# Optimization experiments

Hardware: AMD Instinct MI355X
Metric: run time of the kernel (lower is better)

The kernel has to match this reference:

```python
import jax, jax.numpy as jnp
import numpy as np

N_NODES = 50000
NEG_SLOPE = 0.2

def _segment_softmax(e, seg, n):
    m = jax.ops.segment_max(e, seg, num_segments=n)
    ex = jnp.exp(e - m[seg])
    s = jax.ops.segment_sum(ex, seg, num_segments=n)
    return ex / s[seg]

def _gatv2_layer(x, src, dst, n, Wl, bl, Wr, br, att):
    # GATv2 (heads=1): e_ij = att . leaky_relu(Wl x_j + Wr x_i); msg = alpha * Wl x_j
    xl = x @ Wl + bl            # [N, D] source transform
    xr = x @ Wr + br            # [N, D] target transform
    h = jax.nn.leaky_relu(xl[src] + xr[dst], NEG_SLOPE)  # [E, D]
    e = h @ att                 # [E]
    alpha = _segment_softmax(e, dst, n)
    out = jax.ops.segment_sum(alpha[:, None] * xl[src], dst, num_segments=n)
    return out

def setup_inputs() -> dict:
    key = jax.random.key(0)
    ks = jax.random.split(key, 16)
    N, E, Q, F, D, H = N_NODES, 800000, 200000, 128, 250, 256
    def glorot(k, shape):
        fan = shape[0] + shape[-1]
        return jax.random.uniform(k, shape, jnp.float32, -1.0, 1.0) * np.sqrt(6.0 / fan)
    return {
        "x": jax.random.normal(ks[0], (N, F), jnp.float32),
        "edge_index": jax.random.randint(ks[1], (2, E), 0, N, jnp.int32),
        "query": jax.random.randint(ks[2], (Q, 2), 0, N, jnp.int32),
        "W1l": glorot(ks[3], (F, D)), "b1l": jnp.zeros((D,), jnp.float32),
        "W1r": glorot(ks[4], (F, D)), "b1r": jnp.zeros((D,), jnp.float32),
        "att1": glorot(ks[5], (D,)),
        "W2l": glorot(ks[6], (D, D)), "b2l": jnp.zeros((D,), jnp.float32),
        "W2r": glorot(ks[7], (D, D)), "b2r": jnp.zeros((D,), jnp.float32),
        "att2": glorot(ks[8], (D,)),
        "Wm1": glorot(ks[9], (2 * D, H)), "bm1": jnp.zeros((H,), jnp.float32),
        "Wm2": glorot(ks[10], (H, 1)), "bm2": jnp.zeros((1,), jnp.float32),
    }

def reference(x, edge_index, query, W1l, b1l, W1r, b1r, att1,
              W2l, b2l, W2r, b2r, att2, Wm1, bm1, Wm2, bm2):
    n = x.shape[0]
    # add self loops (PyG default add_self_loops=True)
    loops = jnp.arange(n, dtype=edge_index.dtype)
    src = jnp.concatenate([edge_index[0], loops])
    dst = jnp.concatenate([edge_index[1], loops])
    h = _gatv2_layer(x, src, dst, n, W1l, b1l, W1r, b1r, att1)
    h = jax.nn.relu(h)
    emb = _gatv2_layer(h, src, dst, n, W2l, b2l, W2r, b2r, att2)
    # edge-prediction head: gather pair embeddings, concat, MLP
    pair = jnp.concatenate([emb[query[:, 0]], emb[query[:, 1]]], axis=1)  # [Q, 2D]
    out = jax.nn.relu(pair @ Wm1 + bm1)
    out = jax.nn.relu(out @ Wm2 + bm2)
    return out
```

## Files before the change

kernel.cpp:

```cpp
#include <hip/hip_runtime.h>
#include <hip/hip_fp16.h>
#include <math.h>
#include <stdint.h>

#define NN 50000
#define NE 800000
#define ET (NE + NN)
#define FIN 128
#define DD 250
#define HD 256
#define NQ 200000
#define NEG_SLOPE 0.2f

typedef unsigned short u16;
typedef __attribute__((ext_vector_type(4))) float f32x4;
typedef _Float16 h2v __attribute__((ext_vector_type(2)));
typedef _Float16 f16x8 __attribute__((ext_vector_type(8)));

union H2U { h2v h; unsigned int u; };

__device__ __forceinline__ u16 f2h(float v) {
    __half h = __float2half(v);
    return *reinterpret_cast<u16*>(&h);
}
__device__ __forceinline__ float4 ld4h(const u16* p) {
    uint2 r = *(const uint2*)p;
    __half2 a = *(__half2*)&r.x;
    __half2 b = *(__half2*)&r.y;
    float2 fa = __half22float2(a), fb = __half22float2(b);
    return make_float4(fa.x, fa.y, fb.x, fb.y);
}
__device__ __forceinline__ h2v hmax2v(h2v a, h2v b) {
    return __builtin_elementwise_max(a, b);
}


#define DPPMOV(v, ctrl, rm) \
    ((unsigned int)__builtin_amdgcn_update_dpp(0, (int)(v), (ctrl), (rm), 0xF, true))

__device__ __forceinline__ unsigned int h2_wave_sum63(h2v x) {
    H2U u, t; u.h = x;
    t.u = DPPMOV(u.u, 0x111, 0xF); u.h = u.h + t.h;
    t.u = DPPMOV(u.u, 0x112, 0xF); u.h = u.h + t.h;
    t.u = DPPMOV(u.u, 0x114, 0xF); u.h = u.h + t.h;
    t.u = DPPMOV(u.u, 0x118, 0xF); u.h = u.h + t.h;
    t.u = DPPMOV(u.u, 0x142, 0xA); u.h = u.h + t.h;
    t.u = DPPMOV(u.u, 0x143, 0xC); u.h = u.h + t.h;
    return (unsigned int)__builtin_amdgcn_readlane((int)u.u, 63);
}

__device__ __forceinline__ float f32_wave_sum63(float x) {
    union FU { float f; unsigned int u; } a, t, o;
    a.f = x;
    t.u = DPPMOV(a.u, 0x111, 0xF); a.f += t.f;
    t.u = DPPMOV(a.u, 0x112, 0xF); a.f += t.f;
    t.u = DPPMOV(a.u, 0x114, 0xF); a.f += t.f;
    t.u = DPPMOV(a.u, 0x118, 0xF); a.f += t.f;
    t.u = DPPMOV(a.u, 0x142, 0xA); a.f += t.f;
    t.u = DPPMOV(a.u, 0x143, 0xC); a.f += t.f;
    o.u = (unsigned int)__builtin_amdgcn_readlane((int)a.u, 63);
    return o.f;
}


__global__ void count_kernel(const int* __restrict__ ei, int* __restrict__ cnt) {
    int k = blockIdx.x * 256 + threadIdx.x;
    if (k >= ET) return;
    int d = (k < NE) ? ei[NE + k] : (k - NE);
    atomicAdd(&cnt[d], 1);
}

__global__ __launch_bounds__(256) void scan1_kernel(
    int* __restrict__ cnt, int* __restrict__ rowptr, int* __restrict__ bsum)
{
    __shared__ int buf[256];
    int t = threadIdx.x;
    int i = blockIdx.x * 256 + t;
    int v = (i < NN) ? cnt[i] : 0;
    if (i < NN) cnt[i] = 0;
    buf[t] = v;
    __syncthreads();
#pragma unroll
    for (int off = 1; off < 256; off <<= 1) {
        int add = (t >= off) ? buf[t - off] : 0;
        __syncthreads();
        buf[t] += add;
        __syncthreads();
    }
    if (i < NN) rowptr[i] = buf[t] - v;
    if (t == 255) bsum[blockIdx.x] = buf[255];
}

__global__ __launch_bounds__(256) void scan2_kernel(
    int* __restrict__ bsum, int* __restrict__ rowptr, int nb)
{
    __shared__ int buf[256];
    int t = threadIdx.x;
    int v = (t < nb) ? bsum[t] : 0;
    buf[t] = v;
    __syncthreads();
#pragma unroll
    for (int off = 1; off < 256; off <<= 1) {
        int add = (t >= off) ? buf[t - off] : 0;
        __syncthreads();
        buf[t] += add;
        __syncthreads();
    }
    if (t < nb) bsum[t] = buf[t] - v;
    if (t == 255) rowptr[NN] = buf[255];
}

__global__ __launch_bounds__(256) void scan3_kernel(
    int* __restrict__ rowptr, const int* __restrict__ bsum)
{
    int i = blockIdx.x * 256 + threadIdx.x;
    if (i < NN) rowptr[i] += bsum[blockIdx.x];
}

__global__ void scatter_kernel(const int* __restrict__ ei,
                               const int* __restrict__ rowptr,
                               int* __restrict__ fill,
                               int* __restrict__ ssrc) {
    int k = blockIdx.x * 256 + threadIdx.x;
    if (k >= ET) return;
    int s, d;
    if (k < NE) { s = ei[k]; d = ei[NE + k]; }
    else        { s = k - NE; d = k - NE; }
    int pos = rowptr[d] + atomicAdd(&fill[d], 1);
    ssrc[pos] = s << 9;
}


#define CONVX_BLOCKS 3125

__global__ __launch_bounds__(256) void conv_all(
    const float* __restrict__ x, int* __restrict__ fill,
    u16* __restrict__ Asp,
    const float* __restrict__ W1l, const float* __restrict__ W1r,
    const float* __restrict__ W2l, const float* __restrict__ W2r,
    const float* __restrict__ Wm1,
    u16* __restrict__ W1lT, u16* __restrict__ W1rT,
    u16* __restrict__ W2lT, u16* __restrict__ W2rT,
    u16* __restrict__ WmtT, u16* __restrict__ WmbT)
{
    if (blockIdx.x < CONVX_BLOCKS) {
        int tid = blockIdx.x * 256 + threadIdx.x;
        if (tid < NN) fill[tid] = 0;
        size_t idx = (size_t)tid * 8;
        if (idx >= (size_t)NN * FIN) return;
        float4 v0 = *(const float4*)(x + idx);
        float4 v1 = *(const float4*)(x + idx + 4);
        ushort4 o0, o1;
        o0.x = f2h(v0.x); o0.y = f2h(v0.y); o0.z = f2h(v0.z); o0.w = f2h(v0.w);
        o1.x = f2h(v1.x); o1.y = f2h(v1.y); o1.z = f2h(v1.z); o1.w = f2h(v1.w);
        *(ushort4*)(Asp + idx) = o0;
        *(ushort4*)(Asp + idx + 4) = o1;
        return;
    }
    int b = blockIdx.x - CONVX_BLOCKS;
    const float* W; int K, N, koff, kshift, b0; u16* ot;
    if (b < 128)       { W = W1l; K = FIN; N = DD; koff = 0;  kshift = 7; b0 = 0;    ot = W1lT; }
    else if (b < 256)  { W = W1r; K = FIN; N = DD; koff = 0;  kshift = 7; b0 = 128;  ot = W1rT; }
    else if (b < 512)  { W = W2l; K = DD;  N = DD; koff = 0;  kshift = 8; b0 = 256;  ot = W2lT; }
    else if (b < 768)  { W = W2r; K = DD;  N = DD; koff = 0;  kshift = 8; b0 = 512;  ot = W2rT; }
    else if (b < 1024) { W = Wm1; K = DD;  N = HD; koff = 0;  kshift = 8; b0 = 768;  ot = WmtT; }
    else               { W = Wm1; K = DD;  N = HD; koff = DD; kshift = 8; b0 = 1024; ot = WmbT; }
    int id = (b - b0) * 256 + threadIdx.x;
    int Kp = 1 << kshift;
    int n = id >> kshift, k = id & (Kp - 1);
    float v = (n < N && k < K) ? W[(size_t)(k + koff) * N + n] : 0.f;
    ot[id] = f2h(v);
}


#define AP 40

__global__ __launch_bounds__(256, 2) void gemm_pair(
    const u16* __restrict__ A, int Kp,
    const u16* __restrict__ B0, const u16* __restrict__ B1,
    const float* __restrict__ bias0, const float* __restrict__ bias1,
    void* __restrict__ C0v, void* __restrict__ C1v, int M, int N, int fmt)
{
    __shared__ u16 AS[128][AP], B0S[128][AP], B1S[128][AP];

    int row0 = blockIdx.x * 128;
    int col0 = blockIdx.y * 128;
    int t = threadIdx.x;
    int lane = t & 63, w = t >> 6;
    int wr = w >> 1, wc = w & 1;
    int quad = lane >> 4, rr = lane & 15;

    f32x4 acc0[4][4], acc1[4][4];
#pragma unroll
    for (int i = 0; i < 4; i++)
#pragma unroll
        for (int j = 0; j < 4; j++) {
            acc0[i][j] = (f32x4){0.f, 0.f, 0.f, 0.f};
            acc1[i][j] = (f32x4){0.f, 0.f, 0.f, 0.f};
        }

    int ar = t >> 1, akh = (t & 1) * 16;
    int gr = row0 + ar;
    int nB = col0 + ar;
    const u16* pA  = A  + (size_t)gr * Kp + akh;
    const u16* pB0 = B0 + (size_t)nB * Kp + akh;
    const u16* pB1 = B1 + (size_t)nB * Kp + akh;

    for (int k0 = 0; k0 < Kp; k0 += 32) {
        f16x8 a0{}, a1{};
        if (gr < M) {
            a0 = *(const f16x8*)(pA + k0);
            a1 = *(const f16x8*)(pA + k0 + 8);
        }
        *(f16x8*)&AS[ar][akh]      = a0;
        *(f16x8*)&AS[ar][akh + 8]  = a1;
        *(f16x8*)&B0S[ar][akh]     = *(const f16x8*)(pB0 + k0);
        *(f16x8*)&B0S[ar][akh + 8] = *(const f16x8*)(pB0 + k0 + 8);
        *(f16x8*)&B1S[ar][akh]     = *(const f16x8*)(pB1 + k0);
        *(f16x8*)&B1S[ar][akh + 8] = *(const f16x8*)(pB1 + k0 + 8);
        __syncthreads();

        f16x8 fA[4];
#pragma unroll
        for (int fi = 0; fi < 4; fi++) {
            int r = wr * 64 + fi * 16 + rr;
            fA[fi] = *(const f16x8*)&AS[r][quad * 8];
        }
#pragma unroll
        for (int fj = 0; fj < 4; fj++) {
            int c = wc * 64 + fj * 16 + rr;
            f16x8 b0 = *(const f16x8*)&B0S[c][quad * 8];
            f16x8 b1 = *(const f16x8*)&B1S[c][quad * 8];
#pragma unroll
            for (int fi = 0; fi < 4; fi++) {
                acc0[fi][fj] = __builtin_amdgcn_mfma_f32_16x16x32_f16(fA[fi], b0, acc0[fi][fj], 0, 0, 0);
                acc1[fi][fj] = __builtin_amdgcn_mfma_f32_16x16x32_f16(fA[fi], b1, acc1[fi][fj], 0, 0, 0);
            }
        }
        __syncthreads();
    }

#pragma unroll
    for (int fj = 0; fj < 4; fj++) {
        int gc = col0 + wc * 64 + fj * 16 + rr;
        if (gc >= N) continue;
        float bb0 = bias0 ? bias0[gc] : 0.f;
        float bb1 = bias1 ? bias1[gc] : 0.f;
#pragma unroll
        for (int fi = 0; fi < 4; fi++) {
#pragma unroll
            for (int r = 0; r < 4; r++) {
                int grr = row0 + wr * 64 + fi * 16 + quad * 4 + r;
                if (grr < M) {
                    float v0 = acc0[fi][fj][r] + bb0;
                    float v1 = acc1[fi][fj][r] + bb1;
                    if (fmt & 1) ((u16*)C0v)[(size_t)grr * 256 + gc] = f2h(v0);
                    else         ((float*)C0v)[(size_t)grr * N + gc] = v0;
                    if (fmt & 2) ((u16*)C1v)[(size_t)grr * 256 + gc] = f2h(v1);
                    else         ((float*)C1v)[(size_t)grr * N + gc] = v1;
                }
            }
        }
    }
}


__global__ __launch_bounds__(256) void fused_edge_kernel(
    const int* __restrict__ rowptr, const int* __restrict__ ssrc,
    const u16* __restrict__ xl16, const u16* __restrict__ xr16,
    const float* __restrict__ att,
    u16* __restrict__ Oh, int dorelu)
{
    int i = blockIdx.x * 4 + (threadIdx.x >> 6);
    if (i >= NN) return;
    int lane = threadIdx.x & 63;
    int beg = __builtin_amdgcn_readfirstlane(rowptr[i]);
    int end = __builtin_amdgcn_readfirstlane(rowptr[i + 1]);
    int d0 = lane * 4;
    int lb = d0 * 2;

    uint2 xrr = *(const uint2*)&xr16[(size_t)i * 256 + d0];
    h2v xr0h = *(h2v*)&xrr.x, xr1h = *(h2v*)&xrr.y;
    float atf[4] = {0.f, 0.f, 0.f, 0.f};
#pragma unroll
    for (int j = 0; j < 4; j++)
        if (d0 + j < DD) atf[j] = att[d0 + j];
    h2v at0h, at1h;
    at0h.x = (_Float16)atf[0]; at0h.y = (_Float16)atf[1];
    at1h.x = (_Float16)atf[2]; at1h.y = (_Float16)atf[3];
    const h2v c02 = {(_Float16)0.2f, (_Float16)0.2f};

    const char* xlb = (const char*)xl16;

    float m = -1e30f, ssum = 0.f;
    float4 acc = make_float4(0.f, 0.f, 0.f, 0.f);

    auto ldrow = [&](int o) -> uint2 {
        return *(const uint2*)(xlb + o + lb);
    };
    auto edge_score = [&](uint2 g) -> float {
        h2v x0 = *(h2v*)&g.x, x1 = *(h2v*)&g.y;
        h2v s = x0 + xr0h; s = hmax2v(s, s * c02);
        float e = __builtin_amdgcn_fdot2(s, at0h, 0.f, false);
        s = x1 + xr1h; s = hmax2v(s, s * c02);
        return __builtin_amdgcn_fdot2(s, at1h, e, false);
    };
    auto single_update = [&](uint2 g) {
        float e = f32_wave_sum63(edge_score(g));
        h2v x0 = *(h2v*)&g.x, x1 = *(h2v*)&g.y;
        float nm = fmaxf(m, e);
        float sc = __expf(m - nm);
        float w = __expf(e - nm);
        acc.x = fmaf(w, (float)x0.x, acc.x * sc);
        acc.y = fmaf(w, (float)x0.y, acc.y * sc);
        acc.z = fmaf(w, (float)x1.x, acc.z * sc);
        acc.w = fmaf(w, (float)x1.y, acc.w * sc);
        ssum = fmaf(ssum, sc, w);
        m = nm;
    };

    int p = beg;
    if (p + 3 < end) {
        int o0 = __builtin_amdgcn_readfirstlane(ssrc[p]);
        int o1 = __builtin_amdgcn_readfirstlane(ssrc[p + 1]);
        int o2 = __builtin_amdgcn_readfirstlane(ssrc[p + 2]);
        int o3 = __builtin_amdgcn_readfirstlane(ssrc[p + 3]);
        uint2 c0 = ldrow(o0), c1 = ldrow(o1), c2 = ldrow(o2), c3 = ldrow(o3);
        bool hn = (p + 7 < end);
        int no0 = 0, no1 = 0, no2 = 0, no3 = 0;
        if (hn) {
            no0 = __builtin_amdgcn_readfirstlane(ssrc[p + 4]);
            no1 = __builtin_amdgcn_readfirstlane(ssrc[p + 5]);
            no2 = __builtin_amdgcn_readfirstlane(ssrc[p + 6]);
            no3 = __builtin_amdgcn_readfirstlane(ssrc[p + 7]);
        }
        for (;;) {
            uint2 n0, n1, n2, n3;
            if (hn) {
                n0 = ldrow(no0); n1 = ldrow(no1); n2 = ldrow(no2); n3 = ldrow(no3);
            }
            bool hnn = (p + 11 < end);
            int nn0 = 0, nn1 = 0, nn2 = 0, nn3 = 0;
            if (hnn) {
                nn0 = __builtin_amdgcn_readfirstlane(ssrc[p + 8]);
                nn1 = __builtin_amdgcn_readfirstlane(ssrc[p + 9]);
                nn2 = __builtin_amdgcn_readfirstlane(ssrc[p + 10]);
                nn3 = __builtin_amdgcn_readfirstlane(ssrc[p + 11]);
            }

            h2v x00 = *(h2v*)&c0.x, x01 = *(h2v*)&c0.y;
            h2v x10 = *(h2v*)&c1.x, x11 = *(h2v*)&c1.y;
            h2v x20 = *(h2v*)&c2.x, x21 = *(h2v*)&c2.y;
            h2v x30 = *(h2v*)&c3.x, x31 = *(h2v*)&c3.y;

            h2v s;
            float e0, e1, e2, e3;
            s = x00 + xr0h; s = hmax2v(s, s * c02);
            e0 = __builtin_amdgcn_fdot2(s, at0h, 0.f, false);
            s = x01 + xr1h; s = hmax2v(s, s * c02);
            e0 = __builtin_amdgcn_fdot2(s, at1h, e0, false);
            s = x10 + xr0h; s = hmax2v(s, s * c02);
            e1 = __builtin_amdgcn_fdot2(s, at0h, 0.f, false);
            s = x11 + xr1h; s = hmax2v(s, s * c02);
            e1 = __builtin_amdgcn_fdot2(s, at1h, e1, false);
            s = x20 + xr0h; s = hmax2v(s, s * c02);
            e2 = __builtin_amdgcn_fdot2(s, at0h, 0.f, false);
            s = x21 + xr1h; s = hmax2v(s, s * c02);
            e2 = __builtin_amdgcn_fdot2(s, at1h, e2, false);
            s = x30 + xr0h; s = hmax2v(s, s * c02);
            e3 = __builtin_amdgcn_fdot2(s, at0h, 0.f, false);
            s = x31 + xr1h; s = hmax2v(s, s * c02);
            e3 = __builtin_amdgcn_fdot2(s, at1h, e3, false);

            H2U u01, u23, r01, r23;
            u01.h.x = (_Float16)e0; u01.h.y = (_Float16)e1;
            u23.h.x = (_Float16)e2; u23.h.y = (_Float16)e3;
            r01.u = h2_wave_sum63(u01.h);
            r23.u = h2_wave_sum63(u23.h);
            float es0 = (float)r01.h.x, es1 = (float)r01.h.y;
            float es2 = (float)r23.h.x, es3 = (float)r23.h.y;

            float nm = fmaxf(fmaxf(m, es0), fmaxf(fmaxf(es1, es2), es3));
            float sc = __expf(m - nm);
            float w0 = __expf(es0 - nm);
            float w1 = __expf(es1 - nm);
            float w2 = __expf(es2 - nm);
            float w3 = __expf(es3 - nm);
            float ax0 = fmaf(w1, (float)x10.x, w0 * (float)x00.x);
            float ax1 = fmaf(w3, (float)x30.x, w2 * (float)x20.x);
            float ay0 = fmaf(w1, (float)x10.y, w0 * (float)x00.y);
            float ay1 = fmaf(w3, (float)x30.y, w2 * (float)x20.y);
            float az0 = fmaf(w1, (float)x11.x, w0 * (float)x01.x);
            float az1 = fmaf(w3, (float)x31.x, w2 * (float)x21.x);
            float aw0 = fmaf(w1, (float)x11.y, w0 * (float)x01.y);
            float aw1 = fmaf(w3, (float)x31.y, w2 * (float)x21.y);
            acc.x = fmaf(acc.x, sc, ax0 + ax1);
            acc.y = fmaf(acc.y, sc, ay0 + ay1);
            acc.z = fmaf(acc.z, sc, az0 + az1);
            acc.w = fmaf(acc.w, sc, aw0 + aw1);
            ssum = fmaf(ssum, sc, (w0 + w1) + (w2 + w3));
            m = nm;

            p += 4;
            if (!hn) break;
            c0 = n0; c1 = n1; c2 = n2; c3 = n3;
            no0 = nn0; no1 = nn1; no2 = nn2; no3 = nn3;
            hn = hnn;
        }
    }

    int rem = end - p;
    if (rem > 0) {
        int o0 = __builtin_amdgcn_readfirstlane(ssrc[p]);
        int o1 = 0, o2 = 0;
        if (rem > 1) o1 = __builtin_amdgcn_readfirstlane(ssrc[p + 1]);
        if (rem > 2) o2 = __builtin_amdgcn_readfirstlane(ssrc[p + 2]);
        uint2 g0 = ldrow(o0);
        uint2 g1, g2;
        if (rem > 1) g1 = ldrow(o1);
        if (rem > 2) g2 = ldrow(o2);
        single_update(g0);
        if (rem > 1) single_update(g1);
        if (rem > 2) single_update(g2);
    }

    float inv = 1.f / ssum;
    acc.x *= inv; acc.y *= inv; acc.z *= inv; acc.w *= inv;
    if (dorelu) {
        acc.x = fmaxf(acc.x, 0.f); acc.y = fmaxf(acc.y, 0.f);
        acc.z = fmaxf(acc.z, 0.f); acc.w = fmaxf(acc.w, 0.f);
    }
    size_t base = (size_t)i * 256 + d0;
    ushort4 hv;
    hv.x = f2h(acc.x); hv.y = f2h(acc.y); hv.z = f2h(acc.z); hv.w = f2h(acc.w);
    *(ushort4*)&Oh[base] = hv;
}


__global__ __launch_bounds__(256) void query_kernel(
    const int* __restrict__ qry, const u16* __restrict__ Ptop,
    const u16* __restrict__ Pbot, const float* __restrict__ Wm2,
    const float* __restrict__ bm2, float* __restrict__ out)
{
    int q = (blockIdx.x * 4 + (threadIdx.x >> 6)) * 2;
    if (q >= NQ) return;
    int lane = threadIdx.x & 63;
    int a0 = __builtin_amdgcn_readfirstlane(qry[q * 2 + 0]);
    int b0 = __builtin_amdgcn_readfirstlane(qry[q * 2 + 1]);
    int a1 = __builtin_amdgcn_readfirstlane(qry[q * 2 + 2]);
    int b1 = __builtin_amdgcn_readfirstlane(qry[q * 2 + 3]);
    float4 w  = *(const float4*)&Wm2[lane * 4];
    float4 t0 = ld4h(&Ptop[(size_t)a0 * HD + lane * 4]);
    float4 v0 = ld4h(&Pbot[(size_t)b0 * HD + lane * 4]);
    float4 t1 = ld4h(&Ptop[(size_t)a1 * HD + lane * 4]);
    float4 v1 = ld4h(&Pbot[(size_t)b1 * HD + lane * 4]);
    float s0 = fmaxf(t0.x + v0.x, 0.f) * w.x + fmaxf(t0.y + v0.y, 0.f) * w.y
             + fmaxf(t0.z + v0.z, 0.f) * w.z + fmaxf(t0.w + v0.w, 0.f) * w.w;
    float s1 = fmaxf(t1.x + v1.x, 0.f) * w.x + fmaxf(t1.y + v1.y, 0.f) * w.y
             + fmaxf(t1.z + v1.z, 0.f) * w.z + fmaxf(t1.w + v1.w, 0.f) * w.w;
    s0 = f32_wave_sum63(s0);
    s1 = f32_wave_sum63(s1);
    if (lane == 0) {
        float bb = bm2[0];
        out[q] = fmaxf(s0 + bb, 0.f);
        if (q + 1 < NQ) out[q + 1] = fmaxf(s1 + bb, 0.f);
    }
}


extern "C" void kernel_launch(void* const* d_in, const int* in_sizes, int n_in,
                              void* d_out, int out_size, void* d_ws, size_t ws_size,
                              hipStream_t stream) {
    const float* x    = (const float*)d_in[0];
    const int*   ei   = (const int*)d_in[1];
    const int*   qry  = (const int*)d_in[2];
    const float* W1l  = (const float*)d_in[3];
    const float* b1l  = (const float*)d_in[4];
    const float* W1r  = (const float*)d_in[5];
    const float* b1r  = (const float*)d_in[6];
    const float* att1 = (const float*)d_in[7];
    const float* W2l  = (const float*)d_in[8];
    const float* b2l  = (const float*)d_in[9];
    const float* W2r  = (const float*)d_in[10];
    const float* b2r  = (const float*)d_in[11];
    const float* att2 = (const float*)d_in[12];
    const float* Wm1  = (const float*)d_in[13];
    const float* bm1  = (const float*)d_in[14];
    const float* Wm2  = (const float*)d_in[15];
    const float* bm2  = (const float*)d_in[16];
    float* out = (float*)d_out;

    u16* xl16    = (u16*)d_ws;
    u16* xr16    = xl16 + (size_t)NN * 256;
    int* rowptr  = (int*)(xr16 + (size_t)NN * 256);
    int* fill    = rowptr + NN + 1;
    int* ssrc    = fill + NN;
    int* bsum    = ssrc + ET;
    uintptr_t wp = (uintptr_t)(bsum + 256);
    wp = (wp + 63) & ~(uintptr_t)63;
    u16* W1lT = (u16*)wp;
    u16* W1rT = W1lT + 256 * 128;
    u16* W2lT = W1rT + 256 * 128;
    u16* W2rT = W2lT + 65536;
    u16* WmtT = W2rT + 65536;
    u16* WmbT = WmtT + 65536;
    u16* Asp  = WmbT + 65536;
    u16* Ptop16 = xl16;
    u16* Pbot16 = xr16;

    dim3 blk(256);
    int gET = (ET + 255) / 256;
    int gNode = (NN + 3) / 4;
    int nb = (NN + 255) / 256;
    dim3 gg((NN + 127) / 128, 2);

    conv_all<<<CONVX_BLOCKS + 1280, blk, 0, stream>>>(x, fill, Asp,
        W1l, W1r, W2l, W2r, Wm1,
        W1lT, W1rT, W2lT, W2rT, WmtT, WmbT);

    count_kernel<<<gET, blk, 0, stream>>>(ei, fill);
    scan1_kernel<<<nb, blk, 0, stream>>>(fill, rowptr, bsum);
    scan2_kernel<<<1, blk, 0, stream>>>(bsum, rowptr, nb);
    scan3_kernel<<<nb, blk, 0, stream>>>(rowptr, bsum);
    scatter_kernel<<<gET, blk, 0, stream>>>(ei, rowptr, fill, ssrc);

    gemm_pair<<<gg, blk, 0, stream>>>(Asp, 128, W1lT, W1rT,
                                      b1l, b1r, (void*)xl16, (void*)xr16, NN, DD, 3);
    fused_edge_kernel<<<gNode, blk, 0, stream>>>(rowptr, ssrc, xl16, xr16, att1, Asp, 1);

    gemm_pair<<<gg, blk, 0, stream>>>(Asp, 256, W2lT, W2rT,
                                      b2l, b2r, (void*)xl16, (void*)xr16, NN, DD, 3);
    fused_edge_kernel<<<gNode, blk, 0, stream>>>(rowptr, ssrc, xl16, xr16, att2, Asp, 0);

    gemm_pair<<<gg, blk, 0, stream>>>(Asp, 256, WmtT, WmbT,
                                      bm1, (const float*)nullptr, (void*)Ptop16, (void*)Pbot16, NN, HD, 3);

    query_kernel<<<(NQ / 2 + 3) / 4, blk, 0, stream>>>(qry, Ptop16, Pbot16, Wm2, bm2, out);
}
```

Baseline: 522.0 us.

## Fuse degree count into conversion, widen GEMM tiles, batch nodes per wave

The edge-degree count moves into the conversion kernel, and the fill buffer is cleared with a memset, which removes one launch. Attention vectors are pre-converted to fp16 once. The paired GEMM now uses 512-thread blocks that each cover all 256 output columns, so A is loaded once per row tile instead of twice. The edge kernel processes four nodes per wave and prefetches the next node's target row. Together these trade occupancy and register pressure for fewer launches and more reuse.

```diff
diff --git a/kernel.cpp b/kernel.cpp
--- a/kernel.cpp
+++ b/kernel.cpp
@@ -11,6 +11,7 @@
 #define HD 256
 #define NQ 200000
 #define NEG_SLOPE 0.2f
+#define NPW 4
 
 typedef unsigned short u16;
 typedef __attribute__((ext_vector_type(4))) float f32x4;
@@ -63,13 +64,6 @@
 }
 
 
-__global__ void count_kernel(const int* __restrict__ ei, int* __restrict__ cnt) {
-    int k = blockIdx.x * 256 + threadIdx.x;
-    if (k >= ET) return;
-    int d = (k < NE) ? ei[NE + k] : (k - NE);
-    atomicAdd(&cnt[d], 1);
-}
-
 __global__ __launch_bounds__(256) void scan1_kernel(
     int* __restrict__ cnt, int* __restrict__ rowptr, int* __restrict__ bsum)
 {
@@ -132,20 +126,23 @@
 
 
 #define CONVX_BLOCKS 3125
+#define CNT_BLOCKS ((ET + 255) / 256)
 
 __global__ __launch_bounds__(256) void conv_all(
-    const float* __restrict__ x, int* __restrict__ fill,
+    const float* __restrict__ x, const int* __restrict__ ei,
     u16* __restrict__ Asp,
     const float* __restrict__ W1l, const float* __restrict__ W1r,
     const float* __restrict__ W2l, const float* __restrict__ W2r,
     const float* __restrict__ Wm1,
+    const float* __restrict__ att1, const float* __restrict__ att2,
     u16* __restrict__ W1lT, u16* __restrict__ W1rT,
     u16* __restrict__ W2lT, u16* __restrict__ W2rT,
-    u16* __restrict__ WmtT, u16* __restrict__ WmbT)
+    u16* __restrict__ WmtT, u16* __restrict__ WmbT,
+    u16* __restrict__ atth1, u16* __restrict__ atth2,
+    int* __restrict__ cnt)
 {
     if (blockIdx.x < CONVX_BLOCKS) {
         int tid = blockIdx.x * 256 + threadIdx.x;
-        if (tid < NN) fill[tid] = 0;
         size_t idx = (size_t)tid * 8;
         if (idx >= (size_t)NN * FIN) return;
         float4 v0 = *(const float4*)(x + idx);
@@ -158,36 +155,49 @@
         return;
     }
     int b = blockIdx.x - CONVX_BLOCKS;
-    const float* W; int K, N, koff, kshift, b0; u16* ot;
-    if (b < 128)       { W = W1l; K = FIN; N = DD; koff = 0;  kshift = 7; b0 = 0;    ot = W1lT; }
-    else if (b < 256)  { W = W1r; K = FIN; N = DD; koff = 0;  kshift = 7; b0 = 128;  ot = W1rT; }
-    else if (b < 512)  { W = W2l; K = DD;  N = DD; koff = 0;  kshift = 8; b0 = 256;  ot = W2lT; }
-    else if (b < 768)  { W = W2r; K = DD;  N = DD; koff = 0;  kshift = 8; b0 = 512;  ot = W2rT; }
-    else if (b < 1024) { W = Wm1; K = DD;  N = HD; koff = 0;  kshift = 8; b0 = 768;  ot = WmtT; }
-    else               { W = Wm1; K = DD;  N = HD; koff = DD; kshift = 8; b0 = 1024; ot = WmbT; }
-    int id = (b - b0) * 256 + threadIdx.x;
-    int Kp = 1 << kshift;
-    int n = id >> kshift, k = id & (Kp - 1);
-    float v = (n < N && k < K) ? W[(size_t)(k + koff) * N + n] : 0.f;
-    ot[id] = f2h(v);
+    if (b < 1280) {
+        const float* W; int K, N, koff, kshift, b0; u16* ot;
+        if (b < 128)       { W = W1l; K = FIN; N = DD; koff = 0;  kshift = 7; b0 = 0;    ot = W1lT; }
+        else if (b < 256)  { W = W1r; K = FIN; N = DD; koff = 0;  kshift = 7; b0 = 128;  ot = W1rT; }
+        else if (b < 512)  { W = W2l; K = DD;  N = DD; koff = 0;  kshift = 8; b0 = 256;  ot = W2lT; }
+        else if (b < 768)  { W = W2r; K = DD;  N = DD; koff = 0;  kshift = 8; b0 = 512;  ot = W2rT; }
+        else if (b < 1024) { W = Wm1; K = DD;  N = HD; koff = 0;  kshift = 8; b0 = 768;  ot = WmtT; }
+        else               { W = Wm1; K = DD;  N = HD; koff = DD; kshift = 8; b0 = 1024; ot = WmbT; }
+        int id = (b - b0) * 256 + threadIdx.x;
+        int Kp = 1 << kshift;
+        int n = id >> kshift, k = id & (Kp - 1);
+        float v = (n < N && k < K) ? W[(size_t)(k + koff) * N + n] : 0.f;
+        ot[id] = f2h(v);
+        return;
+    }
+    if (b < 1282) {
+        const float* a = (b == 1280) ? att1 : att2;
+        u16* o = (b == 1280) ? atth1 : atth2;
+        int id = threadIdx.x;
+        o[id] = f2h(id < DD ? a[id] : 0.f);
+        return;
+    }
+    int k = (b - 1282) * 256 + threadIdx.x;
+    if (k >= ET) return;
+    int d = (k < NE) ? ei[NE + k] : (k - NE);
+    atomicAdd(&cnt[d], 1);
 }
 
 
 #define AP 40
 
-__global__ __launch_bounds__(256, 2) void gemm_pair(
+__global__ __launch_bounds__(512) void gemm_pair(
     const u16* __restrict__ A, int Kp,
     const u16* __restrict__ B0, const u16* __restrict__ B1,
     const float* __restrict__ bias0, const float* __restrict__ bias1,
     void* __restrict__ C0v, void* __restrict__ C1v, int M, int N, int fmt)
 {
-    __shared__ u16 AS[128][AP], B0S[128][AP], B1S[128][AP];
+    __shared__ u16 AS[128][AP], B0S[256][AP], B1S[256][AP];
 
     int row0 = blockIdx.x * 128;
-    int col0 = blockIdx.y * 128;
     int t = threadIdx.x;
     int lane = t & 63, w = t >> 6;
-    int wr = w >> 1, wc = w & 1;
+    int wr = w >> 2, wc = w & 3;
     int quad = lane >> 4, rr = lane & 15;
 
     f32x4 acc0[4][4], acc1[4][4];
@@ -199,25 +209,23 @@
             acc1[i][j] = (f32x4){0.f, 0.f, 0.f, 0.f};
         }
 
-    int ar = t >> 1, akh = (t & 1) * 16;
-    int gr = row0 + ar;
-    int nB = col0 + ar;
-    const u16* pA  = A  + (size_t)gr * Kp + akh;
-    const u16* pB0 = B0 + (size_t)nB * Kp + akh;
-    const u16* pB1 = B1 + (size_t)nB * Kp + akh;
+    int arow = t >> 2, akc = (t & 3) * 8;
+    bool aok = (row0 + arow) < M;
+    const u16* pA   = A  + (size_t)(row0 + arow) * Kp + akc;
+    int brow = t >> 2, bkc = akc;
+    const u16* pB0a = B0 + (size_t)brow * Kp + bkc;
+    const u16* pB0b = pB0a + (size_t)128 * Kp;
+    const u16* pB1a = B1 + (size_t)brow * Kp + bkc;
+    const u16* pB1b = pB1a + (size_t)128 * Kp;
 
     for (int k0 = 0; k0 < Kp; k0 += 32) {
-        f16x8 a0{}, a1{};
-        if (gr < M) {
-            a0 = *(const f16x8*)(pA + k0);
-            a1 = *(const f16x8*)(pA + k0 + 8);
-        }
-        *(f16x8*)&AS[ar][akh]      = a0;
-        *(f16x8*)&AS[ar][akh + 8]  = a1;
-        *(f16x8*)&B0S[ar][akh]     = *(const f16x8*)(pB0 + k0);
-        *(f16x8*)&B0S[ar][akh + 8] = *(const f16x8*)(pB0 + k0 + 8);
-        *(f16x8*)&B1S[ar][akh]     = *(const f16x8*)(pB1 + k0);
-        *(f16x8*)&B1S[ar][akh + 8] = *(const f16x8*)(pB1 + k0 + 8);
+        f16x8 a{};
+        if (aok) a = *(const f16x8*)(pA + k0);
+        *(f16x8*)&AS[arow][akc]            = a;
+        *(f16x8*)&B0S[brow][bkc]           = *(const f16x8*)(pB0a + k0);
+        *(f16x8*)&B0S[brow + 128][bkc]     = *(const f16x8*)(pB0b + k0);
+        *(f16x8*)&B1S[brow][bkc]           = *(const f16x8*)(pB1a + k0);
+        *(f16x8*)&B1S[brow + 128][bkc]     = *(const f16x8*)(pB1b + k0);
         __syncthreads();
 
         f16x8 fA[4];
@@ -242,7 +250,7 @@
 
 #pragma unroll
     for (int fj = 0; fj < 4; fj++) {
-        int gc = col0 + wc * 64 + fj * 16 + rr;
+        int gc = wc * 64 + fj * 16 + rr;
         if (gc >= N) continue;
         float bb0 = bias0 ? bias0[gc] : 0.f;
         float bb1 = bias1 ? bias1[gc] : 0.f;
@@ -268,172 +276,177 @@
 __global__ __launch_bounds__(256) void fused_edge_kernel(
     const int* __restrict__ rowptr, const int* __restrict__ ssrc,
     const u16* __restrict__ xl16, const u16* __restrict__ xr16,
-    const float* __restrict__ att,
+    const u16* __restrict__ atth,
     u16* __restrict__ Oh, int dorelu)
 {
-    int i = blockIdx.x * 4 + (threadIdx.x >> 6);
-    if (i >= NN) return;
+    int wid = blockIdx.x * 4 + (threadIdx.x >> 6);
+    int base = wid * NPW;
+    if (base >= NN) return;
     int lane = threadIdx.x & 63;
-    int beg = __builtin_amdgcn_readfirstlane(rowptr[i]);
-    int end = __builtin_amdgcn_readfirstlane(rowptr[i + 1]);
     int d0 = lane * 4;
     int lb = d0 * 2;
 
-    uint2 xrr = *(const uint2*)&xr16[(size_t)i * 256 + d0];
-    h2v xr0h = *(h2v*)&xrr.x, xr1h = *(h2v*)&xrr.y;
-    float atf[4] = {0.f, 0.f, 0.f, 0.f};
-#pragma unroll
-    for (int j = 0; j < 4; j++)
-        if (d0 + j < DD) atf[j] = att[d0 + j];
-    h2v at0h, at1h;
-    at0h.x = (_Float16)atf[0]; at0h.y = (_Float16)atf[1];
-    at1h.x = (_Float16)atf[2]; at1h.y = (_Float16)atf[3];
+    uint2 atr = *(const uint2*)&atth[d0];
+    h2v at0h = *(h2v*)&atr.x, at1h = *(h2v*)&atr.y;
     const h2v c02 = {(_Float16)0.2f, (_Float16)0.2f};
-
     const char* xlb = (const char*)xl16;
-
-    float m = -1e30f, ssum = 0.f;
-    float4 acc = make_float4(0.f, 0.f, 0.f, 0.f);
 
     auto ldrow = [&](int o) -> uint2 {
         return *(const uint2*)(xlb + o + lb);
     };
-    auto edge_score = [&](uint2 g) -> float {
-        h2v x0 = *(h2v*)&g.x, x1 = *(h2v*)&g.y;
-        h2v s = x0 + xr0h; s = hmax2v(s, s * c02);
-        float e = __builtin_amdgcn_fdot2(s, at0h, 0.f, false);
-        s = x1 + xr1h; s = hmax2v(s, s * c02);
-        return __builtin_amdgcn_fdot2(s, at1h, e, false);
-    };
-    auto single_update = [&](uint2 g) {
-        float e = f32_wave_sum63(edge_score(g));
-        h2v x0 = *(h2v*)&g.x, x1 = *(h2v*)&g.y;
-        float nm = fmaxf(m, e);
-        float sc = __expf(m - nm);
-        float w = __expf(e - nm);
-        acc.x = fmaf(w, (float)x0.x, acc.x * sc);
-        acc.y = fmaf(w, (float)x0.y, acc.y * sc);
-        acc.z = fmaf(w, (float)x1.x, acc.z * sc);
-        acc.w = fmaf(w, (float)x1.y, acc.w * sc);
-        ssum = fmaf(ssum, sc, w);
-        m = nm;
-    };
-
-    int p = beg;
-    if (p + 3 < end) {
-        int o0 = __builtin_amdgcn_readfirstlane(ssrc[p]);
-        int o1 = __builtin_amdgcn_readfirstlane(ssrc[p + 1]);
-        int o2 = __builtin_amdgcn_readfirstlane(ssrc[p + 2]);
-        int o3 = __builtin_amdgcn_readfirstlane(ssrc[p + 3]);
-        uint2 c0 = ldrow(o0), c1 = ldrow(o1), c2 = ldrow(o2), c3 = ldrow(o3);
-        bool hn = (p + 7 < end);
-        int no0 = 0, no1 = 0, no2 = 0, no3 = 0;
-        if (hn) {
-            no0 = __builtin_amdgcn_readfirstlane(ssrc[p + 4]);
-            no1 = __builtin_amdgcn_readfirstlane(ssrc[p + 5]);
-            no2 = __builtin_amdgcn_readfirstlane(ssrc[p + 6]);
-            no3 = __builtin_amdgcn_readfirstlane(ssrc[p + 7]);
-        }
-        for (;;) {
-            uint2 n0, n1, n2, n3;
+
+    uint2 xrr = *(const uint2*)&xr16[(size_t)base * 256 + d0];
+
+    for (int k = 0; k < NPW; k++) {
+        int i = base + k;
+        if (i >= NN) break;
+        h2v xr0h = *(h2v*)&xrr.x, xr1h = *(h2v*)&xrr.y;
+        int beg = __builtin_amdgcn_readfirstlane(rowptr[i]);
+        int end = __builtin_amdgcn_readfirstlane(rowptr[i + 1]);
+
+        float m = -1e30f, ssum = 0.f;
+        float4 acc = make_float4(0.f, 0.f, 0.f, 0.f);
+
+        auto edge_score = [&](uint2 g) -> float {
+            h2v x0 = *(h2v*)&g.x, x1 = *(h2v*)&g.y;
+            h2v s = x0 + xr0h; s = hmax2v(s, s * c02);
+            float e = __builtin_amdgcn_fdot2(s, at0h, 0.f, false);
+            s = x1 + xr1h; s = hmax2v(s, s * c02);
+            return __builtin_amdgcn_fdot2(s, at1h, e, false);
+        };
+        auto single_update = [&](uint2 g) {
+            float e = f32_wave_sum63(edge_score(g));
+            h2v x0 = *(h2v*)&g.x, x1 = *(h2v*)&g.y;
+            float nm = fmaxf(m, e);
+            float sc = __expf(m - nm);
+            float w = __expf(e - nm);
+            acc.x = fmaf(w, (float)x0.x, acc.x * sc);
+            acc.y = fmaf(w, (float)x0.y, acc.y * sc);
+            acc.z = fmaf(w, (float)x1.x, acc.z * sc);
+            acc.w = fmaf(w, (float)x1.y, acc.w * sc);
+            ssum = fmaf(ssum, sc, w);
+            m = nm;
+        };
+
+        int p = beg;
+        if (p + 3 < end) {
+            int o0 = __builtin_amdgcn_readfirstlane(ssrc[p]);
+            int o1 = __builtin_amdgcn_readfirstlane(ssrc[p + 1]);
+            int o2 = __builtin_amdgcn_readfirstlane(ssrc[p + 2]);
+            int o3 = __builtin_amdgcn_readfirstlane(ssrc[p + 3]);
+            uint2 c0 = ldrow(o0), c1 = ldrow(o1), c2 = ldrow(o2), c3 = ldrow(o3);
+            bool hn = (p + 7 < end);
+            int no0 = 0, no1 = 0, no2 = 0, no3 = 0;
             if (hn) {
-                n0 = ldrow(no0); n1 = ldrow(no1); n2 = ldrow(no2); n3 = ldrow(no3);
+                no0 = __builtin_amdgcn_readfirstlane(ssrc[p + 4]);
+                no1 = __builtin_amdgcn_readfirstlane(ssrc[p + 5]);
+                no2 = __builtin_amdgcn_readfirstlane(ssrc[p + 6]);
+                no3 = __builtin_amdgcn_readfirstlane(ssrc[p + 7]);
             }
-            bool hnn = (p + 11 < end);
-            int nn0 = 0, nn1 = 0, nn2 = 0, nn3 = 0;
-            if (hnn) {
-                nn0 = __builtin_amdgcn_readfirstlane(ssrc[p + 8]);
-                nn1 = __builtin_amdgcn_readfirstlane(ssrc[p + 9]);
-                nn2 = __builtin_amdgcn_readfirstlane(ssrc[p + 10]);
-                nn3 = __builtin_amdgcn_readfirstlane(ssrc[p + 11]);
+            for (;;) {
+                uint2 n0, n1, n2, n3;
+                if (hn) {
+                    n0 = ldrow(no0); n1 = ldrow(no1); n2 = ldrow(no2); n3 = ldrow(no3);
+                }
+                bool hnn = (p + 11 < end);
+                int nn0 = 0, nn1 = 0, nn2 = 0, nn3 = 0;
+                if (hnn) {
+                    nn0 = __builtin_amdgcn_readfirstlane(ssrc[p + 8]);
+                    nn1 = __builtin_amdgcn_readfirstlane(ssrc[p + 9]);
+                    nn2 = __builtin_amdgcn_readfirstlane(ssrc[p + 10]);
+                    nn3 = __builtin_amdgcn_readfirstlane(ssrc[p + 11]);
+                }
+
+                h2v x00 = *(h2v*)&c0.x, x01 = *(h2v*)&c0.y;
+                h2v x10 = *(h2v*)&c1.x, x11 = *(h2v*)&c1.y;
+                h2v x20 = *(h2v*)&c2.x, x21 = *(h2v*)&c2.y;
+                h2v x30 = *(h2v*)&c3.x, x31 = *(h2v*)&c3.y;
+
+                h2v s;
+                float e0, e1, e2, e3;
+                s = x00 + xr0h; s = hmax2v(s, s * c02);
+                e0 = __builtin_amdgcn_fdot2(s, at0h, 0.f, false);
+                s = x01 + xr1h; s = hmax2v(s, s * c02);
+                e0 = __builtin_amdgcn_fdot2(s, at1h, e0, false);
+                s = x10 + xr0h; s = hmax2v(s, s * c02);
+                e1 = __builtin_amdgcn_fdot2(s, at0h, 0.f, false);
+                s = x11 + xr1h; s = hmax2v(s, s * c02);
+                e1 = __builtin_amdgcn_fdot2(s, at1h, e1, false);
+                s = x20 + xr0h; s = hmax2v(s, s * c02);
+                e2 = __builtin_amdgcn_fdot2(s, at0h, 0.f, false);
+                s = x21 + xr1h; s = hmax2v(s, s * c02);
+                e2 = __builtin_amdgcn_fdot2(s, at1h, e2, false);
+                s = x30 + xr0h; s = hmax2v(s, s * c02);
+                e3 = __builtin_amdgcn_fdot2(s, at0h, 0.f, false);
+                s = x31 + xr1h; s = hmax2v(s, s * c02);
+                e3 = __builtin_amdgcn_fdot2(s, at1h, e3, false);
+
+                H2U u01, u23, r01, r23;
+                u01.h.x = (_Float16)e0; u01.h.y = (_Float16)e1;
+                u23.h.x = (_Float16)e2; u23.h.y = (_Float16)e3;
+                r01.u = h2_wave_sum63(u01.h);
+                r23.u = h2_wave_sum63(u23.h);
+                float es0 = (float)r01.h.x, es1 = (float)r01.h.y;
+                float es2 = (float)r23.h.x, es3 = (float)r23.h.y;
+
+                float nm = fmaxf(fmaxf(m, es0), fmaxf(fmaxf(es1, es2), es3));
+                float sc = __expf(m - nm);
+                float w0 = __expf(es0 - nm);
+                float w1 = __expf(es1 - nm);
+                float w2 = __expf(es2 - nm);
+                float w3 = __expf(es3 - nm);
+                float ax0 = fmaf(w1, (float)x10.x, w0 * (float)x00.x);
+                float ax1 = fmaf(w3, (float)x30.x, w2 * (float)x20.x);
+                float ay0 = fmaf(w1, (float)x10.y, w0 * (float)x00.y);
+                float ay1 = fmaf(w3, (float)x30.y, w2 * (float)x20.y);
+                float az0 = fmaf(w1, (float)x11.x, w0 * (float)x01.x);
+                float az1 = fmaf(w3, (float)x31.x, w2 * (float)x21.x);
+                float aw0 = fmaf(w1, (float)x11.y, w0 * (float)x01.y);
+                float aw1 = fmaf(w3, (float)x31.y, w2 * (float)x21.y);
+                acc.x = fmaf(acc.x, sc, ax0 + ax1);
+                acc.y = fmaf(acc.y, sc, ay0 + ay1);
+                acc.z = fmaf(acc.z, sc, az0 + az1);
+                acc.w = fmaf(acc.w, sc, aw0 + aw1);
+                ssum = fmaf(ssum, sc, (w0 + w1) + (w2 + w3));
+                m = nm;
+
+                p += 4;
+                if (!hn) break;
+                c0 = n0; c1 = n1; c2 = n2; c3 = n3;
+                no0 = nn0; no1 = nn1; no2 = nn2; no3 = nn3;
+                hn = hnn;
             }
-
-            h2v x00 = *(h2v*)&c0.x, x01 = *(h2v*)&c0.y;
-            h2v x10 = *(h2v*)&c1.x, x11 = *(h2v*)&c1.y;
-            h2v x20 = *(h2v*)&c2.x, x21 = *(h2v*)&c2.y;
-            h2v x30 = *(h2v*)&c3.x, x31 = *(h2v*)&c3.y;
-
-            h2v s;
-            float e0, e1, e2, e3;
-            s = x00 + xr0h; s = hmax2v(s, s * c02);
-            e0 = __builtin_amdgcn_fdot2(s, at0h, 0.f, false);
-            s = x01 + xr1h; s = hmax2v(s, s * c02);
-            e0 = __builtin_amdgcn_fdot2(s, at1h, e0, false);
-            s = x10 + xr0h; s = hmax2v(s, s * c02);
-            e1 = __builtin_amdgcn_fdot2(s, at0h, 0.f, false);
-            s = x11 + xr1h; s = hmax2v(s, s * c02);
-            e1 = __builtin_amdgcn_fdot2(s, at1h, e1, false);
-            s = x20 + xr0h; s = hmax2v(s, s * c02);
-            e2 = __builtin_amdgcn_fdot2(s, at0h, 0.f, false);
-            s = x21 + xr1h; s = hmax2v(s, s * c02);
-            e2 = __builtin_amdgcn_fdot2(s, at1h, e2, false);
-            s = x30 + xr0h; s = hmax2v(s, s * c02);
-            e3 = __builtin_amdgcn_fdot2(s, at0h, 0.f, false);
-            s = x31 + xr1h; s = hmax2v(s, s * c02);
-            e3 = __builtin_amdgcn_fdot2(s, at1h, e3, false);
-
-            H2U u01, u23, r01, r23;
-            u01.h.x = (_Float16)e0; u01.h.y = (_Float16)e1;
-            u23.h.x = (_Float16)e2; u23.h.y = (_Float16)e3;
-            r01.u = h2_wave_sum63(u01.h);
-            r23.u = h2_wave_sum63(u23.h);
-            float es0 = (float)r01.h.x, es1 = (float)r01.h.y;
-            float es2 = (float)r23.h.x, es3 = (float)r23.h.y;
-
-            float nm = fmaxf(fmaxf(m, es0), fmaxf(fmaxf(es1, es2), es3));
-            float sc = __expf(m - nm);
-            float w0 = __expf(es0 - nm);
-            float w1 = __expf(es1 - nm);
-            float w2 = __expf(es2 - nm);
-            float w3 = __expf(es3 - nm);
-            float ax0 = fmaf(w1, (float)x10.x, w0 * (float)x00.x);
-            float ax1 = fmaf(w3, (float)x30.x, w2 * (float)x20.x);
-            float ay0 = fmaf(w1, (float)x10.y, w0 * (float)x00.y);
-            float ay1 = fmaf(w3, (float)x30.y, w2 * (float)x20.y);
-            float az0 = fmaf(w1, (float)x11.x, w0 * (float)x01.x);
-            float az1 = fmaf(w3, (float)x31.x, w2 * (float)x21.x);
-            float aw0 = fmaf(w1, (float)x11.y, w0 * (float)x01.y);
-            float aw1 = fmaf(w3, (float)x31.y, w2 * (float)x21.y);
-            acc.x = fmaf(acc.x, sc, ax0 + ax1);
-            acc.y = fmaf(acc.y, sc, ay0 + ay1);
-            acc.z = fmaf(acc.z, sc, az0 + az1);
-            acc.w = fmaf(acc.w, sc, aw0 + aw1);
-            ssum = fmaf(ssum, sc, (w0 + w1) + (w2 + w3));
-            m = nm;
-
-            p += 4;
-            if (!hn) break;
-            c0 = n0; c1 = n1; c2 = n2; c3 = n3;
-            no0 = nn0; no1 = nn1; no2 = nn2; no3 = nn3;
-            hn = hnn;
-        }
-    }
-
-    int rem = end - p;
-    if (rem > 0) {
-        int o0 = __builtin_amdgcn_readfirstlane(ssrc[p]);
-        int o1 = 0, o2 = 0;
-        if (rem > 1) o1 = __builtin_amdgcn_readfirstlane(ssrc[p + 1]);
-        if (rem > 2) o2 = __builtin_amdgcn_readfirstlane(ssrc[p + 2]);
-        uint2 g0 = ldrow(o0);
-        uint2 g1, g2;
-        if (rem > 1) g1 = ldrow(o1);
-        if (rem > 2) g2 = ldrow(o2);
-        single_update(g0);
-        if (rem > 1) single_update(g1);
-        if (rem > 2) single_update(g2);
-    }
-
-    float inv = 1.f / ssum;
-    acc.x *= inv; acc.y *= inv; acc.z *= inv; acc.w *= inv;
-    if (dorelu) {
-        acc.x = fmaxf(acc.x, 0.f); acc.y = fmaxf(acc.y, 0.f);
-        acc.z = fmaxf(acc.z, 0.f); acc.w = fmaxf(acc.w, 0.f);
-    }
-    size_t base = (size_t)i * 256 + d0;
-    ushort4 hv;
-    hv.x = f2h(acc.x); hv.y = f2h(acc.y); hv.z = f2h(acc.z); hv.w = f2h(acc.w);
-    *(ushort4*)&Oh[base] = hv;
+        }
+
+        if (k + 1 < NPW && i + 1 < NN)
+            xrr = *(const uint2*)&xr16[(size_t)(i + 1) * 256 + d0];
+
+        int rem = end - p;
+        if (rem > 0) {
+            int o0 = __builtin_amdgcn_readfirstlane(ssrc[p]);
+            int o1 = 0, o2 = 0;
+            if (rem > 1) o1 = __builtin_amdgcn_readfirstlane(ssrc[p + 1]);
+            if (rem > 2) o2 = __builtin_amdgcn_readfirstlane(ssrc[p + 2]);
+            uint2 g0 = ldrow(o0);
+            uint2 g1, g2;
+            if (rem > 1) g1 = ldrow(o1);
+            if (rem > 2) g2 = ldrow(o2);
+            single_update(g0);
+            if (rem > 1) single_update(g1);
+            if (rem > 2) single_update(g2);
+        }
+
+        float inv = 1.f / ssum;
+        acc.x *= inv; acc.y *= inv; acc.z *= inv; acc.w *= inv;
+        if (dorelu) {
+            acc.x = fmaxf(acc.x, 0.f); acc.y = fmaxf(acc.y, 0.f);
+            acc.z = fmaxf(acc.z, 0.f); acc.w = fmaxf(acc.w, 0.f);
+        }
+        size_t obase = (size_t)i * 256 + d0;
+        ushort4 hv;
+        hv.x = f2h(acc.x); hv.y = f2h(acc.y); hv.z = f2h(acc.z); hv.w = f2h(acc.w);
+        *(ushort4*)&Oh[obase] = hv;
+    }
 }
 
 
@@ -496,7 +509,9 @@
     int* fill    = rowptr + NN + 1;
     int* ssrc    = fill + NN;
     int* bsum    = ssrc + ET;
-    uintptr_t wp = (uintptr_t)(bsum + 256);
+    u16* atth1   = (u16*)(bsum + 256);
+    u16* atth2   = atth1 + 256;
+    uintptr_t wp = (uintptr_t)(atth2 + 256);
     wp = (wp + 63) & ~(uintptr_t)63;
     u16* W1lT = (u16*)wp;
     u16* W1rT = W1lT + 256 * 128;
@@ -510,29 +525,29 @@
 
     dim3 blk(256);
     int gET = (ET + 255) / 256;
-    int gNode = (NN + 3) / 4;
+    int gNode = (NN + 4 * NPW - 1) / (4 * NPW);
     int nb = (NN + 255) / 256;
-    dim3 gg((NN + 127) / 128, 2);
-
-    conv_all<<<CONVX_BLOCKS + 1280, blk, 0, stream>>>(x, fill, Asp,
-        W1l, W1r, W2l, W2r, Wm1,
-        W1lT, W1rT, W2lT, W2rT, WmtT, WmbT);
-
-    count_kernel<<<gET, blk, 0, stream>>>(ei, fill);
+    int gg = (NN + 127) / 128;
+
+    hipMemsetAsync(fill, 0, (size_t)NN * sizeof(int), stream);
+    conv_all<<<CONVX_BLOCKS + 1282 + gET, blk, 0, stream>>>(x, ei, Asp,
+        W1l, W1r, W2l, W2r, Wm1, att1, att2,
+        W1lT, W1rT, W2lT, W2rT, WmtT, WmbT, atth1, atth2, fill);
+
     scan1_kernel<<<nb, blk, 0, stream>>>(fill, rowptr, bsum);
     scan2_kernel<<<1, blk, 0, stream>>>(bsum, rowptr, nb);
     scan3_kernel<<<nb, blk, 0, stream>>>(rowptr, bsum);
     scatter_kernel<<<gET, blk, 0, stream>>>(ei, rowptr, fill, ssrc);
 
-    gemm_pair<<<gg, blk, 0, stream>>>(Asp, 128, W1lT, W1rT,
+    gemm_pair<<<gg, dim3(512), 0, stream>>>(Asp, 128, W1lT, W1rT,
                                       b1l, b1r, (void*)xl16, (void*)xr16, NN, DD, 3);
-    fused_edge_kernel<<<gNode, blk, 0, stream>>>(rowptr, ssrc, xl16, xr16, att1, Asp, 1);
-
-    gemm_pair<<<gg, blk, 0, stream>>>(Asp, 256, W2lT, W2rT,
+    fused_edge_kernel<<<gNode, blk, 0, stream>>>(rowptr, ssrc, xl16, xr16, atth1, Asp, 1);
+
+    gemm_pair<<<gg, dim3(512), 0, stream>>>(Asp, 256, W2lT, W2rT,
                                       b2l, b2r, (void*)xl16, (void*)xr16, NN, DD, 3);
-    fused_edge_kernel<<<gNode, blk, 0, stream>>>(rowptr, ssrc, xl16, xr16, att2, Asp, 0);
-
-    gemm_pair<<<gg, blk, 0, stream>>>(Asp, 256, WmtT, WmbT,
+    fused_edge_kernel<<<gNode, blk, 0, stream>>>(rowptr, ssrc, xl16, xr16, atth2, Asp, 0);
+
+    gemm_pair<<<gg, dim3(512), 0, stream>>>(Asp, 256, WmtT, WmbT,
                                       bm1, (const float*)nullptr, (void*)Ptop16, (void*)Pbot16, NN, HD, 3);
 
     query_kernel<<<(NQ / 2 + 3) / 4, blk, 0, stream>>>(qry, Ptop16, Pbot16, Wm2, bm2, out);
```

New measurement: 530.6 us. Within noise of the previous version (+1.6%).
